# Optimization experiments

Measured on AMD Instinct MI355X. Metric: run time of the kernel, lower is better.

## Reference

```python
import jax, jax.numpy as jnp
import numpy as np

SEQ_LEN = 512
VOCAB = 32000
EMB = 512
HID = 1024
NUM_CLASSES = 32000
BATCH = 64


def _lstm_layer(x, w_ih, w_hh, b_ih, b_hh):
    # x: [B, T, D_in]; PyTorch gate order i, f, g, o; weights [4H, D]
    B = x.shape[0]
    H = w_hh.shape[1]
    # precompute input projections for all timesteps: [T, B, 4H]
    xg = jnp.einsum('btd,gd->tbg', x, w_ih) + (b_ih + b_hh)

    def step(carry, xt):
        h, c = carry
        gates = xt + h @ w_hh.T  # [B, 4H]
        i, f, g, o = jnp.split(gates, 4, axis=-1)
        i = jax.nn.sigmoid(i)
        f = jax.nn.sigmoid(f)
        g = jnp.tanh(g)
        o = jax.nn.sigmoid(o)
        c = f * c + i * g
        h = o * jnp.tanh(c)
        return (h, c), h

    h0 = jnp.zeros((B, H), dtype=x.dtype)
    c0 = jnp.zeros((B, H), dtype=x.dtype)
    _, hs = jax.lax.scan(step, (h0, c0), xg)  # hs: [T, B, H]
    return jnp.transpose(hs, (1, 0, 2))  # [B, T, H]


def setup_inputs() -> dict:
    key = jax.random.key(0)
    ks = jax.random.split(key, 12)
    s_e = 1.0 / np.sqrt(EMB)
    s_h = 1.0 / np.sqrt(HID)
    inp = {
        'features': jax.random.randint(ks[0], (BATCH, SEQ_LEN), 0, VOCAB, dtype=jnp.int64)
            if jax.config.jax_enable_x64 else jax.random.randint(ks[0], (BATCH, SEQ_LEN), 0, VOCAB, dtype=jnp.int32),
        'emb': jax.random.normal(ks[1], (VOCAB + 1, EMB), jnp.float32),
        'w_ih0': jax.random.uniform(ks[2], (4 * HID, EMB), jnp.float32, -s_h, s_h),
        'w_hh0': jax.random.uniform(ks[3], (4 * HID, HID), jnp.float32, -s_h, s_h),
        'b_ih0': jax.random.uniform(ks[4], (4 * HID,), jnp.float32, -s_h, s_h),
        'b_hh0': jax.random.uniform(ks[5], (4 * HID,), jnp.float32, -s_h, s_h),
        'w_ih1': jax.random.uniform(ks[6], (4 * HID, HID), jnp.float32, -s_h, s_h),
        'w_hh1': jax.random.uniform(ks[7], (4 * HID, HID), jnp.float32, -s_h, s_h),
        'b_ih1': jax.random.uniform(ks[8], (4 * HID,), jnp.float32, -s_h, s_h),
        'b_hh1': jax.random.uniform(ks[9], (4 * HID,), jnp.float32, -s_h, s_h),
        'fc_w': jax.random.uniform(ks[10], (NUM_CLASSES, HID), jnp.float32, -s_h, s_h),
        'fc_b': jax.random.uniform(ks[11], (NUM_CLASSES,), jnp.float32, -s_h, s_h),
    }
    return inp


def reference(features, emb, w_ih0, w_hh0, b_ih0, b_hh0,
              w_ih1, w_hh1, b_ih1, b_hh1, fc_w, fc_b):
    # seq_lens = sum(features != vocab_size - 1) - 1
    seq_lens = jnp.sum(features != (VOCAB - 1), axis=1) - 1  # [B]
    x = emb[features]  # [B, T, E]
    h1 = _lstm_layer(x, w_ih0, w_hh0, b_ih0, b_hh0)   # [B, T, H]
    h2 = _lstm_layer(h1, w_ih1, w_hh1, b_ih1, b_hh1)  # [B, T, H]
    # gather output at seq_lens per batch row
    last = jnp.take_along_axis(h2, seq_lens[:, None, None].astype(jnp.int32), axis=1)[:, 0]  # [B, H]
    # dropout_rate = 0.0 -> identity
    pred = last @ fc_w.T + fc_b  # [B, num_classes]
    return pred
```

## Files before the change

### kernel.cpp

```cpp
#include <hip/hip_runtime.h>

#define NWG   256
#define NTHR  512
#define TSEQ  512
#define HID   1024
#define NCLS  32000
#define KP1   2056
#define KP0   1544
#define RP    44
#define SPIN_GUARD 50000000u

typedef __attribute__((ext_vector_type(8))) short short8;
typedef __attribute__((ext_vector_type(4))) float floatx4;

struct AB { short8 a[4]; short8 b[2]; };

__device__ __forceinline__ unsigned short f2bf(float f) {
  union { float f; unsigned u; } c; c.f = f;
  unsigned r = c.u + 0x7fffu + ((c.u >> 16) & 1u);
  return (unsigned short)(r >> 16);
}
__device__ __forceinline__ float sigmoidf_(float x) {
  x = fminf(30.f, fmaxf(-30.f, x));
  return 1.f / (1.f + __expf(-x));
}
__device__ __forceinline__ float tanhf_(float x) {
  x = fminf(15.f, fmaxf(-15.f, x));
  float e = __expf(2.f * x);
  return (e - 1.f) / (e + 1.f);
}
__device__ __forceinline__ void st_u32_agent(unsigned* p, unsigned v) {
  __hip_atomic_store(p, v, __ATOMIC_RELAXED, __HIP_MEMORY_SCOPE_AGENT);
}

__device__ __forceinline__ void mfma8(const AB& f, floatx4 (&acc)[4][2]) {
#pragma unroll
  for (int mt = 0; mt < 4; ++mt)
#pragma unroll
    for (int nt = 0; nt < 2; ++nt)
      acc[mt][nt] = __builtin_amdgcn_mfma_f32_16x16x32_bf16(f.a[mt], f.b[nt], acc[mt][nt], 0, 0, 0);
}

template <int NKT, int KPAD>
__device__ __forceinline__ void gemm_step(
    int kb, int kx, int keo, int lm,
    const unsigned short* const (&xb)[4], const unsigned short* const (&hb)[4],
    const unsigned short* wl, floatx4 (&acc)[4][2])
{
  AB f0, f1;
  auto ld = [&](AB& f, int kt) {
    const int k = kb + kt * 32;
    const int off = k + keo;
#pragma unroll
    for (int nt = 0; nt < 2; ++nt)
      f.b[nt] = *reinterpret_cast<const short8*>(wl + (nt * 16 + lm) * KPAD + off);
    const bool inx = k < kx;
#pragma unroll
    for (int mt = 0; mt < 4; ++mt)
      f.a[mt] = *reinterpret_cast<const short8*>((inx ? xb[mt] : hb[mt]) + off);
  };
  ld(f0, 0);
#pragma unroll
  for (int kt = 0; kt + 2 < NKT; kt += 2) {
    ld(f1, kt + 1);
    mfma8(f0, acc);
    ld(f0, kt + 2);
    mfma8(f1, acc);
  }
  ld(f1, NKT - 1);
  mfma8(f0, acc);
  mfma8(f1, acc);
}

__global__ void __launch_bounds__(NTHR, 1)
lstm_kernel(const int* __restrict__ feat,
            const float* __restrict__ emb,
            const float* __restrict__ wih0, const float* __restrict__ whh0,
            const float* __restrict__ bih0, const float* __restrict__ bhh0,
            const float* __restrict__ wih1, const float* __restrict__ whh1,
            const float* __restrict__ bih1, const float* __restrict__ bhh1,
            const float* __restrict__ fcw, const float* __restrict__ fcb,
            float* __restrict__ out,
            unsigned* __restrict__ bar)
{
  const int tid  = threadIdx.x;
  const int wg   = blockIdx.x;
  const int wave = tid >> 6;
  const int lane = tid & 63;
  const int quad = lane >> 4;
  const int lm   = lane & 15;
  const int keo  = quad * 8;

  unsigned short* sc   = (unsigned short*)out;
  unsigned short* h0   = sc;
  unsigned short* h1   = sc + 524288;
  unsigned short* lh   = sc + 655360;
  unsigned short* xbuf = sc + 720896;

  const int layer = (wg >= 128) ? 1 : 0;
  const int wl_id = wg & 127;
  const int jb = wl_id * 8;

  __shared__ unsigned short wlds[32 * KP1];
  __shared__ float red[4][32][RP];
  __shared__ int   sl[64];

  {
    const float* wih = layer ? wih1 : wih0;
    const float* whh = layer ? whh1 : whh0;
    const int KX   = layer ? 1024 : 512;
    const int KTOT = layer ? 2048 : 1536;
    const int KPAD = layer ? KP1 : KP0;
    for (int r = 0; r < 32; ++r) {
      const int gr = (r >> 3) * HID + jb + (r & 7);
      for (int e4 = tid; e4 < (KTOT >> 2); e4 += NTHR) {
        const int k = e4 * 4;
        float4 v = (k < KX) ? *(const float4*)(wih + (size_t)gr * KX + k)
                            : *(const float4*)(whh + (size_t)gr * 1024 + (k - KX));
        ushort4 u; u.x = f2bf(v.x); u.y = f2bf(v.y); u.z = f2bf(v.z); u.w = f2bf(v.w);
        *(ushort4*)(wlds + r * KPAD + k) = u;
      }
    }
    if (layer && tid < 64) {
      int cnt = 0;
      const int* fr = feat + tid * TSEQ;
      for (int k = 0; k < TSEQ; k += 4)
        cnt += (fr[k] != 31999) + (fr[k + 1] != 31999) +
               (fr[k + 2] != 31999) + (fr[k + 3] != 31999);
      int v = cnt - 1; if (v < 0) v = 0;
      sl[tid] = v;
    }
  }
  __syncthreads();

  float bsum[4];
  float cv[2] = {0.f, 0.f};
  int   slv[2] = {0, 0};
  const int jl_c = tid & 7;
  const int bl_c = tid >> 3;
  if (tid < 256) {
    const float* bih = layer ? bih1 : bih0;
    const float* bhh = layer ? bhh1 : bhh0;
    const int gj = jb + jl_c;
#pragma unroll
    for (int g = 0; g < 4; ++g) bsum[g] = bih[g * HID + gj] + bhh[g * HID + gj];
    if (layer) { slv[0] = sl[bl_c]; slv[1] = sl[32 + bl_c]; }
  }

  if (!layer && tid < 256) {
    const int b = wl_id >> 1;
    const int off = (wl_id & 1) * 256 + tid;
    unsigned xv = f2bf(emb[(size_t)feat[b * TSEQ + 0] * 512 + off]);
    unsigned ov = (unsigned)__shfl_xor((int)xv, 1, 64);
    if ((tid & 1) == 0)
      st_u32_agent((unsigned*)(xbuf + b * 512 + off), xv | (ov << 16));
  }

  auto spin_ge = [&](int idx, unsigned need) {
    unsigned gcnt = 0;
    while (__hip_atomic_load(&bar[idx], __ATOMIC_RELAXED, __HIP_MEMORY_SCOPE_AGENT) < need) {
      __builtin_amdgcn_s_sleep(1);
      if (++gcnt > SPIN_GUARD) break;
    }
  };

  unsigned tgt = 0;
  auto sync_group = [&](int cbase, int c2, int cflag, int oflag, unsigned oneed) {
    ++tgt;
    __builtin_amdgcn_s_waitcnt(0);
    __syncthreads();
    if (tid == 0) {
      unsigned old = __hip_atomic_fetch_add(&bar[cbase + (wg & 7) * 32], 1u,
                                            __ATOMIC_RELAXED, __HIP_MEMORY_SCOPE_AGENT);
      if (old == tgt * 16u - 1u) {
        unsigned mo = __hip_atomic_fetch_add(&bar[c2], 1u,
                                             __ATOMIC_RELAXED, __HIP_MEMORY_SCOPE_AGENT);
        if (mo == tgt * 8u - 1u)
          __hip_atomic_store(&bar[cflag], tgt, __ATOMIC_RELAXED, __HIP_MEMORY_SCOPE_AGENT);
      }
      spin_ge(cflag, tgt);
      if (oneed) spin_ge(oflag, oneed);
      __builtin_amdgcn_fence(__ATOMIC_ACQUIRE, "agent");
    }
    __syncthreads();
  };

  auto sync_all = [&]() {
    __builtin_amdgcn_s_waitcnt(0);
    __syncthreads();
    if (tid == 0) {
      unsigned old = __hip_atomic_fetch_add(&bar[640 + (wg & 7) * 32], 1u,
                                            __ATOMIC_RELAXED, __HIP_MEMORY_SCOPE_AGENT);
      if (old == 31u) {
        unsigned mo = __hip_atomic_fetch_add(&bar[896], 1u,
                                             __ATOMIC_RELAXED, __HIP_MEMORY_SCOPE_AGENT);
        if (mo == 7u)
          __hip_atomic_store(&bar[928], 1u, __ATOMIC_RELAXED, __HIP_MEMORY_SCOPE_AGENT);
      }
      spin_ge(928, 1u);
    }
    __syncthreads();
  };

  auto reduce_cell = [&](floatx4 (&acc)[4][2], unsigned short* hw, int t) {
#pragma unroll
    for (int h = 0; h < 2; ++h) {
      if (wave < 4) {
#pragma unroll
        for (int mi = 0; mi < 2; ++mi)
#pragma unroll
          for (int nt = 0; nt < 2; ++nt)
#pragma unroll
            for (int r = 0; r < 4; ++r)
              red[wave][mi * 16 + quad * 4 + r][nt * 16 + lm] = acc[2 * h + mi][nt][r];
      }
      __syncthreads();
      if (wave >= 4) {
#pragma unroll
        for (int mi = 0; mi < 2; ++mi)
#pragma unroll
          for (int nt = 0; nt < 2; ++nt)
#pragma unroll
            for (int r = 0; r < 4; ++r)
              red[wave - 4][mi * 16 + quad * 4 + r][nt * 16 + lm] += acc[2 * h + mi][nt][r];
      }
      __syncthreads();
      if (tid < 256) {
        const int b = h * 32 + bl_c;
        float g0 = bsum[0], g1 = bsum[1], g2 = bsum[2], g3 = bsum[3];
#pragma unroll
        for (int v = 0; v < 4; ++v) {
          g0 += red[v][bl_c][jl_c];
          g1 += red[v][bl_c][8 + jl_c];
          g2 += red[v][bl_c][16 + jl_c];
          g3 += red[v][bl_c][24 + jl_c];
        }
        const float ig = sigmoidf_(g0);
        const float fg = sigmoidf_(g1);
        const float gg = tanhf_(g2);
        const float og = sigmoidf_(g3);
        const float cn = fg * cv[h] + ig * gg;
        cv[h] = cn;
        const float hn = og * tanhf_(cn);
        unsigned my = f2bf(hn);
        unsigned ov = (unsigned)__shfl_xor((int)my, 1, 64);
        if ((tid & 1) == 0) {
          const unsigned packed = my | (ov << 16);
          st_u32_agent((unsigned*)(hw + b * HID + jb + jl_c), packed);
          if (layer && t == slv[h])
            st_u32_agent((unsigned*)(lh + b * HID + jb + jl_c), packed);
        }
      }
      if (h == 0) __syncthreads();
    }
  };

  if (!layer) {
    sync_group(0, 256, 288, 608, 0u);
    for (int t = 0; t < TSEQ; ++t) {
      if (t + 1 < TSEQ && tid < 256) {
        const int b = wl_id >> 1;
        const int off = (wl_id & 1) * 256 + tid;
        unsigned xv = f2bf(emb[(size_t)feat[b * TSEQ + (t + 1)] * 512 + off]);
        unsigned ov = (unsigned)__shfl_xor((int)xv, 1, 64);
        if ((tid & 1) == 0)
          st_u32_agent((unsigned*)(xbuf + ((t + 1) & 1) * 32768 + b * 512 + off), xv | (ov << 16));
      }
      const unsigned short* xq  = xbuf + (size_t)(t & 1) * 32768;
      const unsigned short* h0r = h0 + (size_t)((t + 7) & 7) * 65536;
      const unsigned short* xb[4]; const unsigned short* hb[4];
#pragma unroll
      for (int mt = 0; mt < 4; ++mt) {
        const int row = mt * 16 + lm;
        xb[mt] = xq + row * 512;
        hb[mt] = h0r + row * HID - 512;
      }
      unsigned short* hw = h0 + (size_t)(t & 7) * 65536;

      floatx4 acc[4][2];
#pragma unroll
      for (int mt = 0; mt < 4; ++mt)
#pragma unroll
        for (int nt = 0; nt < 2; ++nt)
          acc[mt][nt] = (floatx4){0.f, 0.f, 0.f, 0.f};
      gemm_step<6, KP0>(wave * 192, 512, keo, lm, xb, hb, wlds, acc);
      reduce_cell(acc, hw, t);

      const unsigned need1 = (t == TSEQ - 1) ? (unsigned)TSEQ
                                             : (unsigned)((t > 6) ? (t - 6) : 0);
      sync_group(0, 256, 288, 608, need1);
    }
  } else {
    if (tid == 0) {
      spin_ge(288, 2u);
      __builtin_amdgcn_fence(__ATOMIC_ACQUIRE, "agent");
    }
    __syncthreads();
    for (int t = 0; t < TSEQ; ++t) {
      const unsigned short* h0r = h0 + (size_t)(t & 7) * 65536;
      const unsigned short* h1r = h1 + (size_t)((t + 1) & 1) * 65536;
      const unsigned short* xb[4]; const unsigned short* hb[4];
#pragma unroll
      for (int mt = 0; mt < 4; ++mt) {
        const int row = mt * 16 + lm;
        xb[mt] = h0r + row * HID;
        hb[mt] = h1r + row * HID - 1024;
      }
      unsigned short* hw = h1 + (size_t)(t & 1) * 65536;

      floatx4 acc[4][2];
#pragma unroll
      for (int mt = 0; mt < 4; ++mt)
#pragma unroll
        for (int nt = 0; nt < 2; ++nt)
          acc[mt][nt] = (floatx4){0.f, 0.f, 0.f, 0.f};
      gemm_step<8, KP1>(wave * 256, 1024, keo, lm, xb, hb, wlds, acc);
      reduce_cell(acc, hw, t);

      const unsigned need0 = (t < TSEQ - 1) ? (unsigned)(t + 3) : 0u;
      sync_group(320, 576, 608, 288, need0);
    }
  }

  const int colbase = wg * 125;
  const int col  = colbase + wave * 16 + lm;
  const int colc = (col < NCLS) ? col : (NCLS - 1);
  floatx4 facc[4];
  {
    const unsigned short* ab[4];
#pragma unroll
    for (int mt = 0; mt < 4; ++mt) ab[mt] = lh + (mt * 16 + lm) * HID;
    const float* bb = fcw + (size_t)colc * HID;

#pragma unroll
    for (int mt = 0; mt < 4; ++mt) facc[mt] = (floatx4){0.f, 0.f, 0.f, 0.f};

    short8 a0[4], a1[4], b0, b1;
    auto ld = [&](short8 (&A)[4], short8& B, int kbase) {
      const int off = kbase + keo;
      float4 v0 = *(const float4*)(bb + off);
      float4 v1 = *(const float4*)(bb + off + 4);
      short8 bv;
      bv[0] = (short)f2bf(v0.x); bv[1] = (short)f2bf(v0.y);
      bv[2] = (short)f2bf(v0.z); bv[3] = (short)f2bf(v0.w);
      bv[4] = (short)f2bf(v1.x); bv[5] = (short)f2bf(v1.y);
      bv[6] = (short)f2bf(v1.z); bv[7] = (short)f2bf(v1.w);
      B = bv;
#pragma unroll
      for (int mt = 0; mt < 4; ++mt)
        A[mt] = *reinterpret_cast<const short8*>(ab[mt] + off);
    };
    ld(a0, b0, 0);
#pragma unroll
    for (int kt = 0; kt < 30; kt += 2) {
      ld(a1, b1, (kt + 1) * 32);
#pragma unroll
      for (int mt = 0; mt < 4; ++mt)
        facc[mt] = __builtin_amdgcn_mfma_f32_16x16x32_bf16(a0[mt], b0, facc[mt], 0, 0, 0);
      ld(a0, b0, (kt + 2) * 32);
#pragma unroll
      for (int mt = 0; mt < 4; ++mt)
        facc[mt] = __builtin_amdgcn_mfma_f32_16x16x32_bf16(a1[mt], b1, facc[mt], 0, 0, 0);
    }
    ld(a1, b1, 31 * 32);
#pragma unroll
    for (int mt = 0; mt < 4; ++mt)
      facc[mt] = __builtin_amdgcn_mfma_f32_16x16x32_bf16(a0[mt], b0, facc[mt], 0, 0, 0);
#pragma unroll
    for (int mt = 0; mt < 4; ++mt)
      facc[mt] = __builtin_amdgcn_mfma_f32_16x16x32_bf16(a1[mt], b1, facc[mt], 0, 0, 0);
  }

  sync_all();

  if (col < colbase + 125) {
    const float bias = fcb[col];
#pragma unroll
    for (int mt = 0; mt < 4; ++mt)
#pragma unroll
      for (int r = 0; r < 4; ++r) {
        const int row = mt * 16 + quad * 4 + r;
        out[(size_t)row * NCLS + col] = facc[mt][r] + bias;
      }
  }
}

extern "C" void kernel_launch(void* const* d_in, const int* in_sizes, int n_in,
                              void* d_out, int out_size, void* d_ws, size_t ws_size,
                              hipStream_t stream) {
  (void)in_sizes; (void)n_in; (void)out_size; (void)ws_size;
  const int*   feat = (const int*)d_in[0];
  const float* emb  = (const float*)d_in[1];
  const float* wih0 = (const float*)d_in[2];
  const float* whh0 = (const float*)d_in[3];
  const float* bih0 = (const float*)d_in[4];
  const float* bhh0 = (const float*)d_in[5];
  const float* wih1 = (const float*)d_in[6];
  const float* whh1 = (const float*)d_in[7];
  const float* bih1 = (const float*)d_in[8];
  const float* bhh1 = (const float*)d_in[9];
  const float* fcw  = (const float*)d_in[10];
  const float* fcb  = (const float*)d_in[11];
  float*       out  = (float*)d_out;
  unsigned*    bar  = (unsigned*)d_ws;

  hipMemsetAsync(d_out, 0, 1572864, stream);
  hipMemsetAsync(d_ws, 0, 8192, stream);

  void* args[] = { &feat, &emb, &wih0, &whh0, &bih0, &bhh0, &wih1, &whh1,
                   &bih1, &bhh1, &fcw, &fcb, &out, &bar };
  hipLaunchCooperativeKernel((const void*)lstm_kernel, dim3(NWG), dim3(NTHR),
                             args, 0, stream);
}
```

Measured before the change: 6.548 ms.

## Split LSTM step into pre-barrier input GEMM and post-barrier recurrent GEMM with decoupled signaling

Each timestep now computes the input-projection part first (layer 0 reads embeddings directly and converts them to bf16 in-register, which drops the staged xbuf), then waits only on the flags it needs before running the recurrent half. The full group barrier at the end of each step is replaced by an in-workgroup counter and a single signaling wave, so the other waves do not block. The aim is to overlap barrier latency with independent GEMM work and to shorten the critical path between timesteps. In exchange it adds deeper register-resident fragment buffering and more delicate memory-ordering logic. The added sync before the FC stage is needed because the FC reads lh.

```diff
diff --git a/kernel.cpp b/kernel.cpp
--- a/kernel.cpp
+++ b/kernel.cpp
@@ -8,6 +8,8 @@
 #define KP1   2056
 #define KP0   1544
 #define RP    44
+#define F0IDX 288
+#define F1IDX 608
 #define SPIN_GUARD 50000000u
 
 typedef __attribute__((ext_vector_type(8))) short short8;
@@ -42,34 +44,57 @@
 }
 
 template <int NKT, int KPAD>
-__device__ __forceinline__ void gemm_step(
-    int kb, int kx, int keo, int lm,
-    const unsigned short* const (&xb)[4], const unsigned short* const (&hb)[4],
+__device__ __forceinline__ void gemm_deep(
+    int kb, int keo, int lm,
+    const unsigned short* const (&ab)[4],
     const unsigned short* wl, floatx4 (&acc)[4][2])
 {
-  AB f0, f1;
-  auto ld = [&](AB& f, int kt) {
-    const int k = kb + kt * 32;
-    const int off = k + keo;
+  AB f[NKT];
+#pragma unroll
+  for (int kt = 0; kt < NKT; ++kt) {
+    const int off = kb + kt * 32 + keo;
 #pragma unroll
     for (int nt = 0; nt < 2; ++nt)
-      f.b[nt] = *reinterpret_cast<const short8*>(wl + (nt * 16 + lm) * KPAD + off);
-    const bool inx = k < kx;
+      f[kt].b[nt] = *reinterpret_cast<const short8*>(wl + (nt * 16 + lm) * KPAD + off);
 #pragma unroll
     for (int mt = 0; mt < 4; ++mt)
-      f.a[mt] = *reinterpret_cast<const short8*>((inx ? xb[mt] : hb[mt]) + off);
-  };
-  ld(f0, 0);
-#pragma unroll
-  for (int kt = 0; kt + 2 < NKT; kt += 2) {
-    ld(f1, kt + 1);
-    mfma8(f0, acc);
-    ld(f0, kt + 2);
-    mfma8(f1, acc);
-  }
-  ld(f1, NKT - 1);
-  mfma8(f0, acc);
-  mfma8(f1, acc);
+      f[kt].a[mt] = *reinterpret_cast<const short8*>(ab[mt] + off);
+  }
+#pragma unroll
+  for (int kt = 0; kt < NKT; ++kt) mfma8(f[kt], acc);
+}
+
+template <int NKT, int KPAD>
+__device__ __forceinline__ void gemm_emb(
+    int kb, int keo, int lm, int t,
+    const int* __restrict__ feat, const float* __restrict__ emb,
+    const unsigned short* wl, floatx4 (&acc)[4][2])
+{
+  const float* er[4];
+#pragma unroll
+  for (int mt = 0; mt < 4; ++mt)
+    er[mt] = emb + (size_t)feat[(mt * 16 + lm) * TSEQ + t] * 512;
+  AB f[NKT];
+#pragma unroll
+  for (int kt = 0; kt < NKT; ++kt) {
+    const int off = kb + kt * 32 + keo;
+#pragma unroll
+    for (int nt = 0; nt < 2; ++nt)
+      f[kt].b[nt] = *reinterpret_cast<const short8*>(wl + (nt * 16 + lm) * KPAD + off);
+#pragma unroll
+    for (int mt = 0; mt < 4; ++mt) {
+      const float4 v0 = *(const float4*)(er[mt] + off);
+      const float4 v1 = *(const float4*)(er[mt] + off + 4);
+      short8 a;
+      a[0] = (short)f2bf(v0.x); a[1] = (short)f2bf(v0.y);
+      a[2] = (short)f2bf(v0.z); a[3] = (short)f2bf(v0.w);
+      a[4] = (short)f2bf(v1.x); a[5] = (short)f2bf(v1.y);
+      a[6] = (short)f2bf(v1.z); a[7] = (short)f2bf(v1.w);
+      f[kt].a[mt] = a;
+    }
+  }
+#pragma unroll
+  for (int kt = 0; kt < NKT; ++kt) mfma8(f[kt], acc);
 }
 
 __global__ void __launch_bounds__(NTHR, 1)
@@ -91,11 +116,10 @@
   const int lm   = lane & 15;
   const int keo  = quad * 8;
 
-  unsigned short* sc   = (unsigned short*)out;
-  unsigned short* h0   = sc;
-  unsigned short* h1   = sc + 524288;
-  unsigned short* lh   = sc + 655360;
-  unsigned short* xbuf = sc + 720896;
+  unsigned short* sc = (unsigned short*)out;
+  unsigned short* h0 = sc;
+  unsigned short* h1 = sc + 524288;
+  unsigned short* lh = sc + 655360;
 
   const int layer = (wg >= 128) ? 1 : 0;
   const int wl_id = wg & 127;
@@ -104,6 +128,9 @@
   __shared__ unsigned short wlds[32 * KP1];
   __shared__ float red[4][32][RP];
   __shared__ int   sl[64];
+  __shared__ unsigned sdone[2];
+
+  if (tid < 2) sdone[tid] = 0;
 
   {
     const float* wih = layer ? wih1 : wih0;
@@ -147,59 +174,13 @@
     if (layer) { slv[0] = sl[bl_c]; slv[1] = sl[32 + bl_c]; }
   }
 
-  if (!layer && tid < 256) {
-    const int b = wl_id >> 1;
-    const int off = (wl_id & 1) * 256 + tid;
-    unsigned xv = f2bf(emb[(size_t)feat[b * TSEQ + 0] * 512 + off]);
-    unsigned ov = (unsigned)__shfl_xor((int)xv, 1, 64);
-    if ((tid & 1) == 0)
-      st_u32_agent((unsigned*)(xbuf + b * 512 + off), xv | (ov << 16));
-  }
-
-  auto spin_ge = [&](int idx, unsigned need) {
-    unsigned gcnt = 0;
-    while (__hip_atomic_load(&bar[idx], __ATOMIC_RELAXED, __HIP_MEMORY_SCOPE_AGENT) < need) {
+  auto spin_ge = [&](int idx, unsigned need) -> unsigned {
+    unsigned g = 0, v;
+    while ((v = __hip_atomic_load(&bar[idx], __ATOMIC_RELAXED, __HIP_MEMORY_SCOPE_AGENT)) < need) {
       __builtin_amdgcn_s_sleep(1);
-      if (++gcnt > SPIN_GUARD) break;
-    }
-  };
-
-  unsigned tgt = 0;
-  auto sync_group = [&](int cbase, int c2, int cflag, int oflag, unsigned oneed) {
-    ++tgt;
-    __builtin_amdgcn_s_waitcnt(0);
-    __syncthreads();
-    if (tid == 0) {
-      unsigned old = __hip_atomic_fetch_add(&bar[cbase + (wg & 7) * 32], 1u,
-                                            __ATOMIC_RELAXED, __HIP_MEMORY_SCOPE_AGENT);
-      if (old == tgt * 16u - 1u) {
-        unsigned mo = __hip_atomic_fetch_add(&bar[c2], 1u,
-                                             __ATOMIC_RELAXED, __HIP_MEMORY_SCOPE_AGENT);
-        if (mo == tgt * 8u - 1u)
-          __hip_atomic_store(&bar[cflag], tgt, __ATOMIC_RELAXED, __HIP_MEMORY_SCOPE_AGENT);
-      }
-      spin_ge(cflag, tgt);
-      if (oneed) spin_ge(oflag, oneed);
-      __builtin_amdgcn_fence(__ATOMIC_ACQUIRE, "agent");
-    }
-    __syncthreads();
-  };
-
-  auto sync_all = [&]() {
-    __builtin_amdgcn_s_waitcnt(0);
-    __syncthreads();
-    if (tid == 0) {
-      unsigned old = __hip_atomic_fetch_add(&bar[640 + (wg & 7) * 32], 1u,
-                                            __ATOMIC_RELAXED, __HIP_MEMORY_SCOPE_AGENT);
-      if (old == 31u) {
-        unsigned mo = __hip_atomic_fetch_add(&bar[896], 1u,
-                                             __ATOMIC_RELAXED, __HIP_MEMORY_SCOPE_AGENT);
-        if (mo == 7u)
-          __hip_atomic_store(&bar[928], 1u, __ATOMIC_RELAXED, __HIP_MEMORY_SCOPE_AGENT);
-      }
-      spin_ge(928, 1u);
-    }
-    __syncthreads();
+      if (++g > SPIN_GUARD) break;
+    }
+    return v;
   };
 
   auto reduce_cell = [&](floatx4 (&acc)[4][2], unsigned short* hw, int t) {
@@ -255,58 +236,73 @@
     }
   };
 
+  auto finish_step = [&](int t, int cbase, int c2, int cflag) {
+    if (wave < 4) {
+      __builtin_amdgcn_s_waitcnt(0);
+      if (lane == 0)
+        __hip_atomic_fetch_add(&sdone[t & 1], 1u, __ATOMIC_RELAXED, __HIP_MEMORY_SCOPE_WORKGROUP);
+    } else if (wave == 7) {
+      if (lane == 0) {
+        unsigned g = 0;
+        while (__hip_atomic_load(&sdone[t & 1], __ATOMIC_RELAXED, __HIP_MEMORY_SCOPE_WORKGROUP) < 4u)
+          if (++g > SPIN_GUARD) break;
+        __hip_atomic_store(&sdone[t & 1], 0u, __ATOMIC_RELAXED, __HIP_MEMORY_SCOPE_WORKGROUP);
+        const unsigned r = (unsigned)t + 1u;
+        unsigned old = __hip_atomic_fetch_add(&bar[cbase + (wg & 7) * 32], 1u,
+                                              __ATOMIC_RELAXED, __HIP_MEMORY_SCOPE_AGENT);
+        if (old == r * 16u - 1u) {
+          unsigned mo = __hip_atomic_fetch_add(&bar[c2], 1u,
+                                               __ATOMIC_RELAXED, __HIP_MEMORY_SCOPE_AGENT);
+          if (mo == r * 8u - 1u)
+            __hip_atomic_store(&bar[cflag], r, __ATOMIC_RELAXED, __HIP_MEMORY_SCOPE_AGENT);
+        }
+      }
+    }
+  };
+
   if (!layer) {
-    sync_group(0, 256, 288, 608, 0u);
+    unsigned seenOwn = 0, seenRing = 0;
     for (int t = 0; t < TSEQ; ++t) {
-      if (t + 1 < TSEQ && tid < 256) {
-        const int b = wl_id >> 1;
-        const int off = (wl_id & 1) * 256 + tid;
-        unsigned xv = f2bf(emb[(size_t)feat[b * TSEQ + (t + 1)] * 512 + off]);
-        unsigned ov = (unsigned)__shfl_xor((int)xv, 1, 64);
-        if ((tid & 1) == 0)
-          st_u32_agent((unsigned*)(xbuf + ((t + 1) & 1) * 32768 + b * 512 + off), xv | (ov << 16));
-      }
-      const unsigned short* xq  = xbuf + (size_t)(t & 1) * 32768;
-      const unsigned short* h0r = h0 + (size_t)((t + 7) & 7) * 65536;
-      const unsigned short* xb[4]; const unsigned short* hb[4];
-#pragma unroll
-      for (int mt = 0; mt < 4; ++mt) {
-        const int row = mt * 16 + lm;
-        xb[mt] = xq + row * 512;
-        hb[mt] = h0r + row * HID - 512;
-      }
-      unsigned short* hw = h0 + (size_t)(t & 7) * 65536;
-
       floatx4 acc[4][2];
 #pragma unroll
       for (int mt = 0; mt < 4; ++mt)
 #pragma unroll
         for (int nt = 0; nt < 2; ++nt)
           acc[mt][nt] = (floatx4){0.f, 0.f, 0.f, 0.f};
-      gemm_step<6, KP0>(wave * 192, 512, keo, lm, xb, hb, wlds, acc);
+
+      gemm_emb<2, KP0>(wave * 64, keo, lm, t, feat, emb, wlds, acc);
+
+      if (tid == 0) {
+        bool fen = false;
+        if (seenOwn < (unsigned)t) { seenOwn = spin_ge(F0IDX, (unsigned)t); fen = true; }
+        const unsigned nr = (t >= 8) ? (unsigned)(t - 7) : 0u;
+        if (seenRing < nr) seenRing = spin_ge(F1IDX, nr);
+        if (fen) __builtin_amdgcn_fence(__ATOMIC_ACQUIRE, "agent");
+      }
+      __syncthreads();
+
+      const unsigned short* hb[4];
+      const unsigned short* h0r = h0 + (size_t)((t + 7) & 7) * 65536;
+#pragma unroll
+      for (int mt = 0; mt < 4; ++mt) hb[mt] = h0r + (mt * 16 + lm) * HID - 512;
+      gemm_deep<4, KP0>(512 + wave * 128, keo, lm, hb, wlds, acc);
+
+      unsigned short* hw = h0 + (size_t)(t & 7) * 65536;
       reduce_cell(acc, hw, t);
-
-      const unsigned need1 = (t == TSEQ - 1) ? (unsigned)TSEQ
-                                             : (unsigned)((t > 6) ? (t - 6) : 0);
-      sync_group(0, 256, 288, 608, need1);
+      finish_step(t, 0, 256, F0IDX);
     }
   } else {
-    if (tid == 0) {
-      spin_ge(288, 2u);
-      __builtin_amdgcn_fence(__ATOMIC_ACQUIRE, "agent");
-    }
-    __syncthreads();
+    unsigned seenX = 0;
+    unsigned seenOwn = 0;
     for (int t = 0; t < TSEQ; ++t) {
-      const unsigned short* h0r = h0 + (size_t)(t & 7) * 65536;
-      const unsigned short* h1r = h1 + (size_t)((t + 1) & 1) * 65536;
-      const unsigned short* xb[4]; const unsigned short* hb[4];
-#pragma unroll
-      for (int mt = 0; mt < 4; ++mt) {
-        const int row = mt * 16 + lm;
-        xb[mt] = h0r + row * HID;
-        hb[mt] = h1r + row * HID - 1024;
-      }
-      unsigned short* hw = h1 + (size_t)(t & 1) * 65536;
+      const unsigned needX = (unsigned)(t + 1);
+      if (seenX < needX) {
+        unsigned v = 0;
+        if (lane == 0) v = spin_ge(F0IDX, needX);
+        v = (unsigned)__shfl((int)v, 0, 64);
+        seenX = v;
+        __builtin_amdgcn_fence(__ATOMIC_ACQUIRE, "agent");
+      }
 
       floatx4 acc[4][2];
 #pragma unroll
@@ -314,13 +310,52 @@
 #pragma unroll
         for (int nt = 0; nt < 2; ++nt)
           acc[mt][nt] = (floatx4){0.f, 0.f, 0.f, 0.f};
-      gemm_step<8, KP1>(wave * 256, 1024, keo, lm, xb, hb, wlds, acc);
+
+      const unsigned short* xb[4];
+      const unsigned short* h0r = h0 + (size_t)(t & 7) * 65536;
+#pragma unroll
+      for (int mt = 0; mt < 4; ++mt) xb[mt] = h0r + (mt * 16 + lm) * HID;
+      gemm_deep<4, KP1>(wave * 128, keo, lm, xb, wlds, acc);
+
+      if (tid == 0) {
+        if (seenOwn < (unsigned)t) {
+          seenOwn = spin_ge(F1IDX, (unsigned)t);
+          __builtin_amdgcn_fence(__ATOMIC_ACQUIRE, "agent");
+        }
+      }
+      __syncthreads();
+
+      const unsigned short* hb[4];
+      const unsigned short* h1r = h1 + (size_t)((t + 1) & 1) * 65536;
+#pragma unroll
+      for (int mt = 0; mt < 4; ++mt) hb[mt] = h1r + (mt * 16 + lm) * HID - 1024;
+      gemm_deep<4, KP1>(1024 + wave * 128, keo, lm, hb, wlds, acc);
+
+      unsigned short* hw = h1 + (size_t)(t & 1) * 65536;
       reduce_cell(acc, hw, t);
-
-      const unsigned need0 = (t < TSEQ - 1) ? (unsigned)(t + 3) : 0u;
-      sync_group(320, 576, 608, 288, need0);
-    }
-  }
+      finish_step(t, 320, 576, F1IDX);
+    }
+  }
+
+  auto sync_all = [&](unsigned r) {
+    __builtin_amdgcn_s_waitcnt(0);
+    __syncthreads();
+    if (tid == 0) {
+      unsigned old = __hip_atomic_fetch_add(&bar[640 + (wg & 7) * 32], 1u,
+                                            __ATOMIC_RELAXED, __HIP_MEMORY_SCOPE_AGENT);
+      if (old == r * 32u - 1u) {
+        unsigned mo = __hip_atomic_fetch_add(&bar[896], 1u,
+                                             __ATOMIC_RELAXED, __HIP_MEMORY_SCOPE_AGENT);
+        if (mo == r * 8u - 1u)
+          __hip_atomic_store(&bar[928], r, __ATOMIC_RELAXED, __HIP_MEMORY_SCOPE_AGENT);
+      }
+      spin_ge(928, r);
+      __builtin_amdgcn_fence(__ATOMIC_ACQUIRE, "agent");
+    }
+    __syncthreads();
+  };
+
+  sync_all(1);
 
   const int colbase = wg * 125;
   const int col  = colbase + wave * 16 + lm;
@@ -371,7 +406,7 @@
       facc[mt] = __builtin_amdgcn_mfma_f32_16x16x32_bf16(a1[mt], b1, facc[mt], 0, 0, 0);
   }
 
-  sync_all();
+  sync_all(2);
 
   if (col < colbase + 125) {
     const float bias = fcb[col];
@@ -404,7 +439,7 @@
   float*       out  = (float*)d_out;
   unsigned*    bar  = (unsigned*)d_ws;
 
-  hipMemsetAsync(d_out, 0, 1572864, stream);
+  hipMemsetAsync(d_out, 0, 1441792, stream);
   hipMemsetAsync(d_ws, 0, 8192, stream);
 
   void* args[] = { &feat, &emb, &wih0, &whh0, &bih0, &bhh0, &wih1, &whh1,
```

Result: slower. 8.325 ms (+27.1%).
